# Kernel tuning notes

Hardware: AMD Instinct MI355X
Metric: run time of the kernel (lower is better)

Reference implementation:

```python
import jax, jax.numpy as jnp
import numpy as np

EPS = 1e-5  # torch group_norm default
GROUPS = 32


def _nin(t, W, b):
    # torch Nin: einsum('bchw,co->bowh') transposes spatial dims, then adds bias
    return jnp.einsum('bchw,co->bowh', t, W) + b


def setup_inputs() -> dict:
    key = jax.random.key(0)
    ks = jax.random.split(key, 9)
    B, C, N = 16, 512, 32
    x = jax.random.normal(ks[0], (B, C, N, N), jnp.float32)
    sc = 0.02
    Wq = jax.random.normal(ks[1], (C, C), jnp.float32) * sc
    Wk = jax.random.normal(ks[2], (C, C), jnp.float32) * sc
    Wv = jax.random.normal(ks[3], (C, C), jnp.float32) * sc
    Wn = jax.random.normal(ks[4], (C, C), jnp.float32) * sc
    bq = jnp.zeros((1, C, 1, 1), jnp.float32)
    bk = jnp.zeros((1, C, 1, 1), jnp.float32)
    bv = jnp.zeros((1, C, 1, 1), jnp.float32)
    bn = jnp.zeros((1, C, 1, 1), jnp.float32)
    return {"x": x, "Wq": Wq, "bq": bq, "Wk": Wk, "bk": bk,
            "Wv": Wv, "bv": bv, "Wn": Wn, "bn": bn}


def reference(x, Wq, bq, Wk, bk, Wv, bv, Wn, bn):
    B, C, H, W = x.shape
    # GroupNorm(32) with no affine params
    xg = x.reshape(B, GROUPS, -1)
    mu = xg.mean(-1, keepdims=True)
    var = xg.var(-1, keepdims=True)
    h = ((xg - mu) / jnp.sqrt(var + EPS)).reshape(B, C, H, W)
    # Nin projections -> spatially transposed (B, C, W, H)
    q = _nin(h, Wq, bq)
    k = _nin(h, Wk, bk)
    v = _nin(h, Wv, bv)
    # scores s[b,w1,w2,h1,h2] = sum_c q[b,c,w1,h1] k[b,c,w2,h2] * C^-0.5
    s = jnp.einsum('bcwh,bcWH->bwWhH', q, k) * (C ** -0.5)
    # softmax over flat (h1,h2) blocks exactly as the torch reshape does
    s = jax.nn.softmax(s.reshape(B, H, W, H * W), axis=-1).reshape(B, H, W, H, W)
    # torch.einsum('bHWHW, bcWH -> bcWH', w, v) takes the DIAGONAL over the
    # repeated H and W labels: diag[b,i,j] = s[b,i,j,i,j], then elementwise
    # scales v: out[b,c,w,h] = diag[b,h,w] * v[b,c,w,h]
    i = jnp.arange(H)
    j = jnp.arange(W)
    diag = s[:, i[:, None], j[None, :], i[:, None], j[None, :]]  # (B,H,W)
    h2 = v * jnp.swapaxes(diag, 1, 2)[:, None]  # (B,C,W,H)
    out = _nin(h2, Wn, bn)  # transposes back -> (B,C,H,W)
    return x + out
```

## Files before the change

kernel.cpp:

```cpp
#include <hip/hip_runtime.h>
#include <hip/hip_bf16.h>

typedef __attribute__((ext_vector_type(8))) short short8;
typedef __attribute__((ext_vector_type(4))) float floatx4;

#define MFMA16(a, b, c) __builtin_amdgcn_mfma_f32_16x16x32_bf16((a), (b), (c), 0, 0, 0)

__device__ __forceinline__ short f2bf(float f) {
    union { float f; unsigned u; } x; x.f = f;
    unsigned r = (x.u + 0x7fffu + ((x.u >> 16) & 1u)) >> 16;
    return (short)r;
}
__device__ __forceinline__ float bf2f(short s) {
    union { float f; unsigned u; } x; x.u = ((unsigned)(unsigned short)s) << 16;
    return x.f;
}

__device__ __forceinline__ void gl2lds16(const short* g, short* l) {
    void* gv = const_cast<short*>(g);
    __builtin_amdgcn_global_load_lds((__attribute__((address_space(1))) void*)gv,
                                     (__attribute__((address_space(3))) void*)l,
                                     16, 0, 0);
}

__global__ void prep_w(const float* __restrict__ Wq, const float* __restrict__ Wk,
                       const float* __restrict__ Wv, const float* __restrict__ Wn,
                       const float* __restrict__ bq, const float* __restrict__ bk,
                       short* __restrict__ wqb, short* __restrict__ wkb,
                       short* __restrict__ Wtv, short* __restrict__ Wn_t,
                       float* __restrict__ wu, float* __restrict__ wv2,
                       float* __restrict__ cstp) {
    __shared__ float t[32][33];
    __shared__ float cred[4];
    int z = blockIdx.z;
    int o0 = blockIdx.x * 32, c0 = blockIdx.y * 32;
    int lx = threadIdx.x, ly = threadIdx.y;
    int tid = ly * 32 + lx;
    if (z < 2) {
        const float* src = z ? Wk : Wq;
        short* dst = z ? wkb : wqb;
        for (int i = ly; i < 32; i += 8)
            dst[(size_t)(c0 + i) * 512 + o0 + lx] = f2bf(src[(size_t)(c0 + i) * 512 + o0 + lx]);
    } else if (z < 4) {
        const float* src = (z == 2) ? Wv : Wn;
        short* dst = (z == 2) ? (Wtv + (size_t)512 * 512) : Wn_t;
        for (int i = ly; i < 32; i += 8) t[i][lx] = src[(size_t)(c0 + i) * 512 + o0 + lx];
        __syncthreads();
        for (int i = ly; i < 32; i += 8) dst[(size_t)(o0 + i) * 512 + c0 + lx] = f2bf(t[lx][i]);
    } else {
        if (blockIdx.y != 0) return;
        int cb = blockIdx.x * 32;
        int cl = tid >> 3, part = tid & 7;
        float su = 0.f, sv = 0.f;
        const float* wqr = Wq + (size_t)(cb + cl) * 512;
        const float* wkr = Wk + (size_t)(cb + cl) * 512;
        for (int o = part * 64; o < part * 64 + 64; ++o) {
            su += wqr[o] * bk[o];
            sv += wkr[o] * bq[o];
        }
        t[cl][part] = su;
        t[cl][part + 8] = sv;
        float sc = 0.f;
        if (blockIdx.x == 0) sc = bq[tid] * bk[tid] + bq[tid + 256] * bk[tid + 256];
#pragma unroll
        for (int off = 32; off > 0; off >>= 1) sc += __shfl_down(sc, off, 64);
        if ((tid & 63) == 0) cred[tid >> 6] = sc;
        __syncthreads();
        if (part == 0) {
            float a = 0.f, b2 = 0.f;
#pragma unroll
            for (int j = 0; j < 8; ++j) { a += t[cl][j]; b2 += t[cl][j + 8]; }
            wu[cb + cl] = a;
            wv2[cb + cl] = b2;
        }
        if (blockIdx.x == 0 && tid == 0) cstp[0] = cred[0] + cred[1] + cred[2] + cred[3];
    }
}

__global__ __launch_bounds__(256) void g_gemm(const short* __restrict__ A,
                                              const short* __restrict__ B,
                                              short* __restrict__ Out) {
    const int tid = threadIdx.x;
    const int wv = tid >> 6, ln = tid & 63;
    const int m0 = blockIdx.x * 128, n0 = blockIdx.y * 128;
    __shared__ __attribute__((aligned(16))) short As[128 * 32];
    __shared__ __attribute__((aligned(16))) short Bs[128 * 32];
    floatx4 acc[4][4] = {};
    const int wm = (wv >> 1) * 64, wn = (wv & 1) * 64;
    const int fr = ln & 15, fq = ln >> 4;
    for (int kk = 0; kk < 512; kk += 32) {
        __syncthreads();
#pragma unroll
        for (int j = 0; j < 2; ++j) {
            int s = (wv * 2 + j) * 64 + ln;
            int r = s >> 2;
            int q = (s & 3) ^ ((r >> 1) & 3);
            gl2lds16(A + (size_t)(m0 + r) * 512 + kk + q * 8, As + (size_t)(wv * 2 + j) * 512);
            gl2lds16(B + (size_t)(n0 + r) * 512 + kk + q * 8, Bs + (size_t)(wv * 2 + j) * 512);
        }
        __syncthreads();
        short8 af[4], bfr[4];
#pragma unroll
        for (int t = 0; t < 4; ++t) {
            int ra = wm + t * 16 + fr;
            af[t]  = *(const short8*)(As + ra * 32 + ((fq ^ ((ra >> 1) & 3)) * 8));
            int rb = wn + t * 16 + fr;
            bfr[t] = *(const short8*)(Bs + rb * 32 + ((fq ^ ((rb >> 1) & 3)) * 8));
        }
#pragma unroll
        for (int mt = 0; mt < 4; ++mt)
#pragma unroll
            for (int nt = 0; nt < 4; ++nt)
                acc[mt][nt] = MFMA16(af[mt], bfr[nt], acc[mt][nt]);
    }
#pragma unroll
    for (int mt = 0; mt < 4; ++mt)
#pragma unroll
        for (int nt = 0; nt < 4; ++nt) {
            int n = n0 + wn + nt * 16 + fr;
#pragma unroll
            for (int r = 0; r < 4; ++r) {
                int m = m0 + wm + mt * 16 + fq * 4 + r;
                Out[(size_t)m * 512 + n] = f2bf(acc[mt][nt][r]);
            }
        }
}

__global__ __launch_bounds__(256) void groupnorm_k(const float* __restrict__ x,
                                                   short* __restrict__ hnt) {
    int b = blockIdx.x >> 5, g = blockIdx.x & 31;
    const float* xg = x + ((size_t)b * 512 + g * 16) * 1024;
    const float4* xg4 = (const float4*)xg;
    float s = 0.f, ss = 0.f;
    for (int i = threadIdx.x; i < 4096; i += 256) {
        float4 v = xg4[i];
        s  += v.x + v.y + v.z + v.w;
        ss += v.x * v.x + v.y * v.y + v.z * v.z + v.w * v.w;
    }
#pragma unroll
    for (int off = 32; off > 0; off >>= 1) {
        s  += __shfl_down(s,  off, 64);
        ss += __shfl_down(ss, off, 64);
    }
    __shared__ float red[8];
    int w = threadIdx.x >> 6;
    if ((threadIdx.x & 63) == 0) { red[w] = s; red[4 + w] = ss; }
    __syncthreads();
    float S  = red[0] + red[1] + red[2] + red[3];
    float SS = red[4] + red[5] + red[6] + red[7];
    float mean = S * (1.f / 16384.f);
    float var  = SS * (1.f / 16384.f) - mean * mean;
    float rstd = rsqrtf(var + 1e-5f);
    __shared__ __attribute__((aligned(16))) short tile[16 * 1026];
    for (int i = threadIdx.x; i < 4096; i += 256) {
        float4 v = xg4[i];
        int c = i >> 8, p = (i & 255) * 4;
        short* tp = tile + c * 1026 + p;
        tp[0] = f2bf((v.x - mean) * rstd);
        tp[1] = f2bf((v.y - mean) * rstd);
        tp[2] = f2bf((v.z - mean) * rstd);
        tp[3] = f2bf((v.w - mean) * rstd);
    }
    __syncthreads();
    for (int i = threadIdx.x; i < 2048; i += 256) {
        int p = i >> 1, half = i & 1;
        short8 v;
#pragma unroll
        for (int j = 0; j < 8; ++j) v[j] = tile[(half * 8 + j) * 1026 + p];
        *(short8*)(hnt + ((size_t)b * 1024 + p) * 512 + g * 16 + half * 8) = v;
    }
}

__global__ __launch_bounds__(256) void uv_gemv(const short* __restrict__ hnt,
                                               const float* __restrict__ wu,
                                               const float* __restrict__ wv2,
                                               float* __restrict__ u1p,
                                               float* __restrict__ v2p) {
    __shared__ float wus[512], wvs[512];
    for (int i = threadIdx.x; i < 512; i += 256) { wus[i] = wu[i]; wvs[i] = wv2[i]; }
    __syncthreads();
    int wv_ = threadIdx.x >> 6, ln = threadIdx.x & 63;
    int row = blockIdx.x * 4 + wv_;
    int b = row >> 10, p = row & 1023;
    short8 h = *(const short8*)(hnt + (size_t)row * 512 + ln * 8);
    float su = 0.f, sv = 0.f;
#pragma unroll
    for (int j = 0; j < 8; ++j) {
        float hv = bf2f(h[j]);
        su += hv * wus[ln * 8 + j];
        sv += hv * wvs[ln * 8 + j];
    }
#pragma unroll
    for (int off = 32; off > 0; off >>= 1) {
        su += __shfl_down(su, off, 64);
        sv += __shfl_down(sv, off, 64);
    }
    if (ln == 0) {
        int pp = ((p & 31) << 5) | (p >> 5);
        u1p[b * 1024 + pp] = su;
        v2p[b * 1024 + pp] = sv;
    }
}

__global__ __launch_bounds__(256) void tv_gemm(const short* __restrict__ A,
                                               const short* __restrict__ Wt,
                                               const float* __restrict__ bv,
                                               short* __restrict__ T,
                                               short* __restrict__ Vb) {
    const int tid = threadIdx.x;
    const int wv = tid >> 6, ln = tid & 63;
    int sid = blockIdx.x + 8 * (blockIdx.y + 8 * blockIdx.z);
    int xcd = sid & 7, chunk = sid >> 3;
    int bz = xcd * 2 + (chunk >> 6);
    int inner = chunk & 63;
    const int m0 = (inner & 7) * 128, n0 = (inner >> 3) * 128;
    const size_t BS = 1024 * 512;
    const short* Ab = A + (size_t)bz * BS;
    const int tsel = n0 >> 9;
    short* Ob = (tsel ? Vb : T) + (size_t)bz * BS;

    __shared__ __attribute__((aligned(16))) short As[128 * 32];
    __shared__ __attribute__((aligned(16))) short Bs[128 * 32];

    floatx4 acc[4][4] = {};
    const int wm = (wv >> 1) * 64, wn = (wv & 1) * 64;
    const int fr = ln & 15, fq = ln >> 4;

    for (int kk = 0; kk < 512; kk += 32) {
        __syncthreads();
#pragma unroll
        for (int j = 0; j < 2; ++j) {
            int s = (wv * 2 + j) * 64 + ln;
            int r = s >> 2;
            int q = (s & 3) ^ ((r >> 1) & 3);
            gl2lds16(Ab + (size_t)(m0 + r) * 512 + kk + q * 8, As + (size_t)(wv * 2 + j) * 512);
            gl2lds16(Wt + (size_t)(n0 + r) * 512 + kk + q * 8, Bs + (size_t)(wv * 2 + j) * 512);
        }
        __syncthreads();
        short8 af[4], bfr[4];
#pragma unroll
        for (int t = 0; t < 4; ++t) {
            int ra = wm + t * 16 + fr;
            af[t]  = *(const short8*)(As + ra * 32 + ((fq ^ ((ra >> 1) & 3)) * 8));
            int rb = wn + t * 16 + fr;
            bfr[t] = *(const short8*)(Bs + rb * 32 + ((fq ^ ((rb >> 1) & 3)) * 8));
        }
#pragma unroll
        for (int mt = 0; mt < 4; ++mt)
#pragma unroll
            for (int nt = 0; nt < 4; ++nt)
                acc[mt][nt] = MFMA16(af[mt], bfr[nt], acc[mt][nt]);
    }
#pragma unroll
    for (int mt = 0; mt < 4; ++mt)
#pragma unroll
        for (int nt = 0; nt < 4; ++nt) {
            int n = n0 + wn + nt * 16 + fr;
            float bvv = tsel ? bv[n - 512] : 0.0f;
            int nn = n & 511;
#pragma unroll
            for (int r = 0; r < 4; ++r) {
                int m = m0 + wm + mt * 16 + fq * 4 + r;
                Ob[(size_t)m * 512 + nn] = f2bf(acc[mt][nt][r] + bvv);
            }
        }
}

__global__ __launch_bounds__(256, 2) void attn_sm(const short* __restrict__ Tt,
                                                  const short* __restrict__ Hn,
                                                  const float* __restrict__ u1p,
                                                  const float* __restrict__ v2p,
                                                  const float* __restrict__ cstp,
                                                  float* __restrict__ Dm) {
    const int tid = threadIdx.x;
    const int wv = tid >> 6, ln = tid & 63;
    int sid = blockIdx.x + 8 * (blockIdx.y + 4 * blockIdx.z);
    int xcd = sid & 7, chunk = sid >> 3;
    int b = xcd * 2 + (chunk >> 5);
    int inner = chunk & 31;
    const int m0 = (inner & 7) * 128, n0 = (inner >> 3) * 256;
    const short* Tb = Tt + (size_t)b * (1024 * 512);
    const short* Hb = Hn + (size_t)b * (1024 * 512);

    __shared__ __attribute__((aligned(16))) short As[128 * 32];
    __shared__ __attribute__((aligned(16))) short Bs[256 * 32];

    floatx4 acc[4][8] = {};
    const int wm = (wv >> 1) * 64, wn = (wv & 1) * 128;
    const int fr = ln & 15, fq = ln >> 4;

    size_t offA[2], offB[4];
#pragma unroll
    for (int j = 0; j < 2; ++j) {
        int s = (wv * 2 + j) * 64 + ln;
        int r = s >> 2;
        int q = (s & 3) ^ ((r >> 1) & 3);
        int m = m0 + r;
        int pm = ((m & 31) << 5) | (m >> 5);
        offA[j] = (size_t)pm * 512 + q * 8;
    }
#pragma unroll
    for (int j = 0; j < 4; ++j) {
        int s = (wv * 4 + j) * 64 + ln;
        int r = s >> 2;
        int q = (s & 3) ^ ((r >> 1) & 3);
        int m = n0 + r;
        int pm = ((m & 31) << 5) | (m >> 5);
        offB[j] = (size_t)pm * 512 + q * 8;
    }

    for (int kk = 0; kk < 512; kk += 32) {
        __syncthreads();
#pragma unroll
        for (int j = 0; j < 2; ++j)
            gl2lds16(Tb + offA[j] + kk, As + (size_t)(wv * 2 + j) * 512);
#pragma unroll
        for (int j = 0; j < 4; ++j)
            gl2lds16(Hb + offB[j] + kk, Bs + (size_t)(wv * 4 + j) * 512);
        __syncthreads();
        short8 af[4], bfr[8];
#pragma unroll
        for (int t = 0; t < 4; ++t) {
            int ra = wm + t * 16 + fr;
            af[t] = *(const short8*)(As + ra * 32 + ((fq ^ ((ra >> 1) & 3)) * 8));
        }
#pragma unroll
        for (int u = 0; u < 8; ++u) {
            int rb = wn + u * 16 + fr;
            bfr[u] = *(const short8*)(Bs + rb * 32 + ((fq ^ ((rb >> 1) & 3)) * 8));
        }
#pragma unroll
        for (int mt = 0; mt < 4; ++mt)
#pragma unroll
            for (int nt = 0; nt < 8; ++nt)
                acc[mt][nt] = MFMA16(af[mt], bfr[nt], acc[mt][nt]);
    }

    const float scale = 0.04419417382415922f;
    const float cst = cstp[0];
    const int wbase = (m0 + wm) >> 5;
    const int Wbase = (n0 + wn) >> 5;
#pragma unroll
    for (int si = 0; si < 2; ++si) {
#pragma unroll
        for (int sj = 0; sj < 4; ++sj) {
            int wg = wbase + si, Wg = Wbase + sj;
            float tv[16];
            float mx = -3.0e38f;
#pragma unroll
            for (int mi = 0; mi < 2; ++mi)
#pragma unroll
                for (int ni = 0; ni < 2; ++ni) {
                    float vc = v2p[b * 1024 + Wg * 32 + ni * 16 + fr];
#pragma unroll
                    for (int r = 0; r < 4; ++r) {
                        float uc = u1p[b * 1024 + wg * 32 + mi * 16 + fq * 4 + r];
                        float u = (acc[2 * si + mi][2 * sj + ni][r] + uc + vc + cst) * scale;
                        tv[(mi * 2 + ni) * 4 + r] = u;
                        mx = fmaxf(mx, u);
                    }
                }
#pragma unroll
            for (int off = 32; off > 0; off >>= 1) mx = fmaxf(mx, __shfl_xor(mx, off, 64));
            float se = 0.f;
#pragma unroll
            for (int i = 0; i < 16; ++i) se += __expf(tv[i] - mx);
#pragma unroll
            for (int off = 32; off > 0; off >>= 1) se += __shfl_xor(se, off, 64);
            if (fq == ((wg >> 2) & 3) && fr == (Wg & 15)) {
                int mi = wg >> 4, ni = Wg >> 4;
                float numer = tv[(mi * 2 + ni) * 4 + (wg & 3)];
                Dm[((size_t)b * 32 + wg) * 32 + Wg] = __expf(numer - mx) / se;
            }
        }
    }
}

__global__ __launch_bounds__(256) void out_gemm(const short* __restrict__ A,
                                                const short* __restrict__ Wt,
                                                const float* __restrict__ Dm,
                                                const float* __restrict__ bnb,
                                                const float* __restrict__ x,
                                                float* __restrict__ out) {
    const int tid = threadIdx.x;
    const int wv = tid >> 6, ln = tid & 63;
    int sid = blockIdx.x + 8 * (blockIdx.y + 4 * blockIdx.z);
    int xcd = sid & 7, chunk = sid >> 3;
    int b = xcd * 2 + (chunk >> 5);
    int inner = chunk & 31;
    const int m0 = (inner & 7) * 128, n0 = (inner >> 3) * 128;
    const size_t BS = 1024 * 512;
    const short* Ab = A + (size_t)b * BS;

    __shared__ __attribute__((aligned(16))) short As[128 * 32];
    __shared__ __attribute__((aligned(16))) short Bs[128 * 32];

    floatx4 acc[4][4] = {};
    const int wm = (wv >> 1) * 64, wn = (wv & 1) * 64;
    const int fr = ln & 15, fq = ln >> 4;

    for (int kk = 0; kk < 512; kk += 32) {
        __syncthreads();
#pragma unroll
        for (int j = 0; j < 2; ++j) {
            int s = (wv * 2 + j) * 64 + ln;
            int r = s >> 2;
            int q = (s & 3) ^ ((r >> 1) & 3);
            gl2lds16(Ab + (size_t)(m0 + r) * 512 + kk + q * 8, As + (size_t)(wv * 2 + j) * 512);
            gl2lds16(Wt + (size_t)(n0 + r) * 512 + kk + q * 8, Bs + (size_t)(wv * 2 + j) * 512);
        }
        __syncthreads();
        short8 af[4], bfr[4];
#pragma unroll
        for (int t = 0; t < 4; ++t) {
            int ra = wm + t * 16 + fr;
            af[t]  = *(const short8*)(As + ra * 32 + ((fq ^ ((ra >> 1) & 3)) * 8));
            int rb = wn + t * 16 + fr;
            bfr[t] = *(const short8*)(Bs + rb * 32 + ((fq ^ ((rb >> 1) & 3)) * 8));
        }
#pragma unroll
        for (int mt = 0; mt < 4; ++mt)
#pragma unroll
            for (int nt = 0; nt < 4; ++nt)
                acc[mt][nt] = MFMA16(af[mt], bfr[nt], acc[mt][nt]);
    }
#pragma unroll
    for (int mt = 0; mt < 4; ++mt) {
        int mbase = m0 + wm + mt * 16 + fq * 4;
        float4 d4 = *(const float4*)(Dm + (size_t)b * 1024 + mbase);
#pragma unroll
        for (int nt = 0; nt < 4; ++nt) {
            int n = n0 + wn + nt * 16 + fr;
            float bvv = bnb[n];
            size_t base = ((size_t)b * 512 + n) * 1024 + mbase;
            float4 x4 = *(const float4*)(x + base);
            float4 o;
            o.x = x4.x + d4.x * acc[mt][nt][0] + bvv;
            o.y = x4.y + d4.y * acc[mt][nt][1] + bvv;
            o.z = x4.z + d4.z * acc[mt][nt][2] + bvv;
            o.w = x4.w + d4.w * acc[mt][nt][3] + bvv;
            *(float4*)(out + base) = o;
        }
    }
}

extern "C" void kernel_launch(void* const* d_in, const int* in_sizes, int n_in,
                              void* d_out, int out_size, void* d_ws, size_t ws_size,
                              hipStream_t stream) {
    const float* x  = (const float*)d_in[0];
    const float* Wq = (const float*)d_in[1];
    const float* bq = (const float*)d_in[2];
    const float* Wk = (const float*)d_in[3];
    const float* bk = (const float*)d_in[4];
    const float* Wv = (const float*)d_in[5];
    const float* bv = (const float*)d_in[6];
    const float* Wn = (const float*)d_in[7];
    const float* bn = (const float*)d_in[8];
    float* out = (float*)d_out;
    char* ws = (char*)d_ws;

    const size_t WSZ = (size_t)512 * 512 * 2;
    const size_t TSZ = (size_t)16 * 1024 * 512 * 2;
    short* Wtv  = (short*)(ws);
    short* Wn_t = (short*)(ws + 2 * WSZ);
    float* wu   = (float*)(ws + 3 * WSZ);
    float* wv2  = wu + 512;
    float* cstp = wv2 + 512;
    float* u1p  = cstp + 16;
    float* v2p  = u1p + 16384;
    char* base = ws + 3 * WSZ + 139264;
    short* hnt = (short*)(base);
    short* T   = (short*)(base + TSZ);
    short* Vb  = (short*)(base + 2 * TSZ);
    float* Dm  = (float*)(base + 3 * TSZ);
    short* wqb = T;
    short* wkb = T + 512 * 512;

    prep_w<<<dim3(16, 16, 5), dim3(32, 8), 0, stream>>>(
        Wq, Wk, Wv, Wn, bq, bk, wqb, wkb, Wtv, Wn_t, wu, wv2, cstp);
    g_gemm<<<dim3(4, 4, 1), 256, 0, stream>>>(wkb, wqb, Wtv);
    groupnorm_k<<<512, 256, 0, stream>>>(x, hnt);
    uv_gemv<<<4096, 256, 0, stream>>>(hnt, wu, wv2, u1p, v2p);
    tv_gemm<<<dim3(8, 8, 16), 256, 0, stream>>>(hnt, Wtv, bv, T, Vb);
    attn_sm<<<dim3(8, 4, 16), 256, 0, stream>>>(T, hnt, u1p, v2p, cstp, Dm);
    out_gemm<<<dim3(8, 4, 16), 256, 0, stream>>>(Vb, Wn_t, Dm, bn, x, out);
}
```

Measured before the change: 219.5 us.

## Fuse prep kernels and drop max-subtraction in attention softmax

```diff
diff --git a/kernel.cpp b/kernel.cpp
--- a/kernel.cpp
+++ b/kernel.cpp
@@ -23,33 +23,87 @@
                                      16, 0, 0);
 }
 
-__global__ void prep_w(const float* __restrict__ Wq, const float* __restrict__ Wk,
-                       const float* __restrict__ Wv, const float* __restrict__ Wn,
-                       const float* __restrict__ bq, const float* __restrict__ bk,
-                       short* __restrict__ wqb, short* __restrict__ wkb,
-                       short* __restrict__ Wtv, short* __restrict__ Wn_t,
-                       float* __restrict__ wu, float* __restrict__ wv2,
-                       float* __restrict__ cstp) {
+__global__ __launch_bounds__(256) void fused_prep(const float* __restrict__ x,
+                                                  const float* __restrict__ Wq,
+                                                  const float* __restrict__ Wk,
+                                                  const float* __restrict__ Wv,
+                                                  const float* __restrict__ Wn,
+                                                  const float* __restrict__ bq,
+                                                  const float* __restrict__ bk,
+                                                  short* __restrict__ hnt,
+                                                  short* __restrict__ wqb,
+                                                  short* __restrict__ wkb,
+                                                  short* __restrict__ Wtv,
+                                                  short* __restrict__ Wn_t,
+                                                  float* __restrict__ wu,
+                                                  float* __restrict__ wv2,
+                                                  float* __restrict__ cstp) {
+    __shared__ __attribute__((aligned(16))) short tile[16 * 1026];
+    __shared__ float red[8];
     __shared__ float t[32][33];
     __shared__ float cred[4];
-    int z = blockIdx.z;
-    int o0 = blockIdx.x * 32, c0 = blockIdx.y * 32;
-    int lx = threadIdx.x, ly = threadIdx.y;
-    int tid = ly * 32 + lx;
-    if (z < 2) {
-        const float* src = z ? Wk : Wq;
-        short* dst = z ? wkb : wqb;
-        for (int i = ly; i < 32; i += 8)
-            dst[(size_t)(c0 + i) * 512 + o0 + lx] = f2bf(src[(size_t)(c0 + i) * 512 + o0 + lx]);
-    } else if (z < 4) {
-        const float* src = (z == 2) ? Wv : Wn;
-        short* dst = (z == 2) ? (Wtv + (size_t)512 * 512) : Wn_t;
-        for (int i = ly; i < 32; i += 8) t[i][lx] = src[(size_t)(c0 + i) * 512 + o0 + lx];
-        __syncthreads();
-        for (int i = ly; i < 32; i += 8) dst[(size_t)(o0 + i) * 512 + c0 + lx] = f2bf(t[lx][i]);
+    const int bid = blockIdx.x, tid = threadIdx.x;
+
+    if (bid < 512) {
+        int b = bid >> 5, g = bid & 31;
+        const float* xg = x + ((size_t)b * 512 + g * 16) * 1024;
+        const float4* xg4 = (const float4*)xg;
+        float s = 0.f, ss = 0.f;
+        for (int i = tid; i < 4096; i += 256) {
+            float4 v = xg4[i];
+            s  += v.x + v.y + v.z + v.w;
+            ss += v.x * v.x + v.y * v.y + v.z * v.z + v.w * v.w;
+        }
+#pragma unroll
+        for (int off = 32; off > 0; off >>= 1) {
+            s  += __shfl_down(s,  off, 64);
+            ss += __shfl_down(ss, off, 64);
+        }
+        int w = tid >> 6;
+        if ((tid & 63) == 0) { red[w] = s; red[4 + w] = ss; }
+        __syncthreads();
+        float S  = red[0] + red[1] + red[2] + red[3];
+        float SS = red[4] + red[5] + red[6] + red[7];
+        float mean = S * (1.f / 16384.f);
+        float var  = SS * (1.f / 16384.f) - mean * mean;
+        float rstd = rsqrtf(var + 1e-5f);
+        for (int i = tid; i < 4096; i += 256) {
+            float4 v = xg4[i];
+            int c = i >> 8, p = (i & 255) * 4;
+            short* tp = tile + c * 1026 + p;
+            tp[0] = f2bf((v.x - mean) * rstd);
+            tp[1] = f2bf((v.y - mean) * rstd);
+            tp[2] = f2bf((v.z - mean) * rstd);
+            tp[3] = f2bf((v.w - mean) * rstd);
+        }
+        __syncthreads();
+        for (int i = tid; i < 2048; i += 256) {
+            int p = i >> 1, half = i & 1;
+            short8 v;
+#pragma unroll
+            for (int j = 0; j < 8; ++j) v[j] = tile[(half * 8 + j) * 1026 + p];
+            *(short8*)(hnt + ((size_t)b * 1024 + p) * 512 + g * 16 + half * 8) = v;
+        }
+    } else if (bid < 1536) {
+        int tz = bid - 512;
+        int z = tz >> 8, inner = tz & 255;
+        int o0 = (inner & 15) * 32, c0 = (inner >> 4) * 32;
+        int lx = tid & 31, ly = tid >> 5;
+        if (z < 2) {
+            const float* src = z ? Wk : Wq;
+            short* dst = z ? wkb : wqb;
+            for (int i = ly; i < 32; i += 8)
+                dst[(size_t)(c0 + i) * 512 + o0 + lx] = f2bf(src[(size_t)(c0 + i) * 512 + o0 + lx]);
+        } else {
+            const float* src = (z == 2) ? Wv : Wn;
+            short* dst = (z == 2) ? (Wtv + (size_t)512 * 512) : Wn_t;
+            for (int i = ly; i < 32; i += 8) t[i][lx] = src[(size_t)(c0 + i) * 512 + o0 + lx];
+            __syncthreads();
+            for (int i = ly; i < 32; i += 8) dst[(size_t)(o0 + i) * 512 + c0 + lx] = f2bf(t[lx][i]);
+        }
     } else {
-        if (blockIdx.y != 0) return;
-        int cb = blockIdx.x * 32;
+        int bid3 = bid - 1536;
+        int cb = bid3 * 32;
         int cl = tid >> 3, part = tid & 7;
         float su = 0.f, sv = 0.f;
         const float* wqr = Wq + (size_t)(cb + cl) * 512;
@@ -61,7 +115,7 @@
         t[cl][part] = su;
         t[cl][part + 8] = sv;
         float sc = 0.f;
-        if (blockIdx.x == 0) sc = bq[tid] * bk[tid] + bq[tid + 256] * bk[tid + 256];
+        if (bid3 == 0) sc = bq[tid] * bk[tid] + bq[tid + 256] * bk[tid + 256];
 #pragma unroll
         for (int off = 32; off > 0; off >>= 1) sc += __shfl_down(sc, off, 64);
         if ((tid & 63) == 0) cred[tid >> 6] = sc;
@@ -73,132 +127,91 @@
             wu[cb + cl] = a;
             wv2[cb + cl] = b2;
         }
-        if (blockIdx.x == 0 && tid == 0) cstp[0] = cred[0] + cred[1] + cred[2] + cred[3];
-    }
-}
-
-__global__ __launch_bounds__(256) void g_gemm(const short* __restrict__ A,
-                                              const short* __restrict__ B,
-                                              short* __restrict__ Out) {
+        if (bid3 == 0 && tid == 0) cstp[0] = cred[0] + cred[1] + cred[2] + cred[3];
+    }
+}
+
+__global__ __launch_bounds__(256) void fused_gu(const short* __restrict__ wkb,
+                                                const short* __restrict__ wqb,
+                                                short* __restrict__ Wtv,
+                                                const short* __restrict__ hnt,
+                                                const float* __restrict__ wu,
+                                                const float* __restrict__ wv2,
+                                                float* __restrict__ u1p,
+                                                float* __restrict__ v2p) {
+    __shared__ __attribute__((aligned(16))) short As[128 * 32];
+    __shared__ __attribute__((aligned(16))) short Bs[128 * 32];
     const int tid = threadIdx.x;
     const int wv = tid >> 6, ln = tid & 63;
-    const int m0 = blockIdx.x * 128, n0 = blockIdx.y * 128;
-    __shared__ __attribute__((aligned(16))) short As[128 * 32];
-    __shared__ __attribute__((aligned(16))) short Bs[128 * 32];
-    floatx4 acc[4][4] = {};
-    const int wm = (wv >> 1) * 64, wn = (wv & 1) * 64;
-    const int fr = ln & 15, fq = ln >> 4;
-    for (int kk = 0; kk < 512; kk += 32) {
-        __syncthreads();
-#pragma unroll
-        for (int j = 0; j < 2; ++j) {
-            int s = (wv * 2 + j) * 64 + ln;
-            int r = s >> 2;
-            int q = (s & 3) ^ ((r >> 1) & 3);
-            gl2lds16(A + (size_t)(m0 + r) * 512 + kk + q * 8, As + (size_t)(wv * 2 + j) * 512);
-            gl2lds16(B + (size_t)(n0 + r) * 512 + kk + q * 8, Bs + (size_t)(wv * 2 + j) * 512);
-        }
-        __syncthreads();
-        short8 af[4], bfr[4];
-#pragma unroll
-        for (int t = 0; t < 4; ++t) {
-            int ra = wm + t * 16 + fr;
-            af[t]  = *(const short8*)(As + ra * 32 + ((fq ^ ((ra >> 1) & 3)) * 8));
-            int rb = wn + t * 16 + fr;
-            bfr[t] = *(const short8*)(Bs + rb * 32 + ((fq ^ ((rb >> 1) & 3)) * 8));
+
+    if (blockIdx.x < 16) {
+        const int m0 = (blockIdx.x & 3) * 128, n0 = (blockIdx.x >> 2) * 128;
+        floatx4 acc[4][4] = {};
+        const int wm = (wv >> 1) * 64, wn = (wv & 1) * 64;
+        const int fr = ln & 15, fq = ln >> 4;
+        for (int kk = 0; kk < 512; kk += 32) {
+            __syncthreads();
+#pragma unroll
+            for (int j = 0; j < 2; ++j) {
+                int s = (wv * 2 + j) * 64 + ln;
+                int r = s >> 2;
+                int q = (s & 3) ^ ((r >> 1) & 3);
+                gl2lds16(wkb + (size_t)(m0 + r) * 512 + kk + q * 8, As + (size_t)(wv * 2 + j) * 512);
+                gl2lds16(wqb + (size_t)(n0 + r) * 512 + kk + q * 8, Bs + (size_t)(wv * 2 + j) * 512);
+            }
+            __syncthreads();
+            short8 af[4], bfr[4];
+#pragma unroll
+            for (int t = 0; t < 4; ++t) {
+                int ra = wm + t * 16 + fr;
+                af[t]  = *(const short8*)(As + ra * 32 + ((fq ^ ((ra >> 1) & 3)) * 8));
+                int rb = wn + t * 16 + fr;
+                bfr[t] = *(const short8*)(Bs + rb * 32 + ((fq ^ ((rb >> 1) & 3)) * 8));
+            }
+#pragma unroll
+            for (int mt = 0; mt < 4; ++mt)
+#pragma unroll
+                for (int nt = 0; nt < 4; ++nt)
+                    acc[mt][nt] = MFMA16(af[mt], bfr[nt], acc[mt][nt]);
         }
 #pragma unroll
         for (int mt = 0; mt < 4; ++mt)
 #pragma unroll
-            for (int nt = 0; nt < 4; ++nt)
-                acc[mt][nt] = MFMA16(af[mt], bfr[nt], acc[mt][nt]);
-    }
-#pragma unroll
-    for (int mt = 0; mt < 4; ++mt)
-#pragma unroll
-        for (int nt = 0; nt < 4; ++nt) {
-            int n = n0 + wn + nt * 16 + fr;
-#pragma unroll
-            for (int r = 0; r < 4; ++r) {
-                int m = m0 + wm + mt * 16 + fq * 4 + r;
-                Out[(size_t)m * 512 + n] = f2bf(acc[mt][nt][r]);
-            }
-        }
-}
-
-__global__ __launch_bounds__(256) void groupnorm_k(const float* __restrict__ x,
-                                                   short* __restrict__ hnt) {
-    int b = blockIdx.x >> 5, g = blockIdx.x & 31;
-    const float* xg = x + ((size_t)b * 512 + g * 16) * 1024;
-    const float4* xg4 = (const float4*)xg;
-    float s = 0.f, ss = 0.f;
-    for (int i = threadIdx.x; i < 4096; i += 256) {
-        float4 v = xg4[i];
-        s  += v.x + v.y + v.z + v.w;
-        ss += v.x * v.x + v.y * v.y + v.z * v.z + v.w * v.w;
-    }
-#pragma unroll
-    for (int off = 32; off > 0; off >>= 1) {
-        s  += __shfl_down(s,  off, 64);
-        ss += __shfl_down(ss, off, 64);
-    }
-    __shared__ float red[8];
-    int w = threadIdx.x >> 6;
-    if ((threadIdx.x & 63) == 0) { red[w] = s; red[4 + w] = ss; }
-    __syncthreads();
-    float S  = red[0] + red[1] + red[2] + red[3];
-    float SS = red[4] + red[5] + red[6] + red[7];
-    float mean = S * (1.f / 16384.f);
-    float var  = SS * (1.f / 16384.f) - mean * mean;
-    float rstd = rsqrtf(var + 1e-5f);
-    __shared__ __attribute__((aligned(16))) short tile[16 * 1026];
-    for (int i = threadIdx.x; i < 4096; i += 256) {
-        float4 v = xg4[i];
-        int c = i >> 8, p = (i & 255) * 4;
-        short* tp = tile + c * 1026 + p;
-        tp[0] = f2bf((v.x - mean) * rstd);
-        tp[1] = f2bf((v.y - mean) * rstd);
-        tp[2] = f2bf((v.z - mean) * rstd);
-        tp[3] = f2bf((v.w - mean) * rstd);
-    }
-    __syncthreads();
-    for (int i = threadIdx.x; i < 2048; i += 256) {
-        int p = i >> 1, half = i & 1;
-        short8 v;
-#pragma unroll
-        for (int j = 0; j < 8; ++j) v[j] = tile[(half * 8 + j) * 1026 + p];
-        *(short8*)(hnt + ((size_t)b * 1024 + p) * 512 + g * 16 + half * 8) = v;
-    }
-}
-
-__global__ __launch_bounds__(256) void uv_gemv(const short* __restrict__ hnt,
-                                               const float* __restrict__ wu,
-                                               const float* __restrict__ wv2,
-                                               float* __restrict__ u1p,
-                                               float* __restrict__ v2p) {
-    __shared__ float wus[512], wvs[512];
-    for (int i = threadIdx.x; i < 512; i += 256) { wus[i] = wu[i]; wvs[i] = wv2[i]; }
-    __syncthreads();
-    int wv_ = threadIdx.x >> 6, ln = threadIdx.x & 63;
-    int row = blockIdx.x * 4 + wv_;
-    int b = row >> 10, p = row & 1023;
-    short8 h = *(const short8*)(hnt + (size_t)row * 512 + ln * 8);
-    float su = 0.f, sv = 0.f;
-#pragma unroll
-    for (int j = 0; j < 8; ++j) {
-        float hv = bf2f(h[j]);
-        su += hv * wus[ln * 8 + j];
-        sv += hv * wvs[ln * 8 + j];
-    }
-#pragma unroll
-    for (int off = 32; off > 0; off >>= 1) {
-        su += __shfl_down(su, off, 64);
-        sv += __shfl_down(sv, off, 64);
-    }
-    if (ln == 0) {
-        int pp = ((p & 31) << 5) | (p >> 5);
-        u1p[b * 1024 + pp] = su;
-        v2p[b * 1024 + pp] = sv;
+            for (int nt = 0; nt < 4; ++nt) {
+                int n = n0 + wn + nt * 16 + fr;
+                const int fq2 = ln >> 4;
+#pragma unroll
+                for (int r = 0; r < 4; ++r) {
+                    int m = m0 + wm + mt * 16 + fq2 * 4 + r;
+                    Wtv[(size_t)m * 512 + n] = f2bf(acc[mt][nt][r]);
+                }
+            }
+    } else {
+        const float4* wu4 = (const float4*)wu;
+        const float4* wv4 = (const float4*)wv2;
+        float4 u0 = wu4[ln * 2], u1 = wu4[ln * 2 + 1];
+        float4 v0 = wv4[ln * 2], v1 = wv4[ln * 2 + 1];
+        int base_row = (blockIdx.x - 16) * 32 + wv * 8;
+#pragma unroll
+        for (int rr = 0; rr < 8; ++rr) {
+            int row = base_row + rr;
+            int b = row >> 10, p = row & 1023;
+            short8 h = *(const short8*)(hnt + (size_t)row * 512 + ln * 8);
+            float su = bf2f(h[0]) * u0.x + bf2f(h[1]) * u0.y + bf2f(h[2]) * u0.z + bf2f(h[3]) * u0.w
+                     + bf2f(h[4]) * u1.x + bf2f(h[5]) * u1.y + bf2f(h[6]) * u1.z + bf2f(h[7]) * u1.w;
+            float sv = bf2f(h[0]) * v0.x + bf2f(h[1]) * v0.y + bf2f(h[2]) * v0.z + bf2f(h[3]) * v0.w
+                     + bf2f(h[4]) * v1.x + bf2f(h[5]) * v1.y + bf2f(h[6]) * v1.z + bf2f(h[7]) * v1.w;
+#pragma unroll
+            for (int off = 32; off > 0; off >>= 1) {
+                su += __shfl_down(su, off, 64);
+                sv += __shfl_down(sv, off, 64);
+            }
+            if (ln == 0) {
+                int pp = ((p & 31) << 5) | (p >> 5);
+                u1p[b * 1024 + pp] = su;
+                v2p[b * 1024 + pp] = sv;
+            }
+        }
     }
 }
 
@@ -345,8 +358,8 @@
 #pragma unroll
         for (int sj = 0; sj < 4; ++sj) {
             int wg = wbase + si, Wg = Wbase + sj;
-            float tv[16];
-            float mx = -3.0e38f;
+            float ex[16];
+            float se = 0.f;
 #pragma unroll
             for (int mi = 0; mi < 2; ++mi)
 #pragma unroll
@@ -355,22 +368,16 @@
 #pragma unroll
                     for (int r = 0; r < 4; ++r) {
                         float uc = u1p[b * 1024 + wg * 32 + mi * 16 + fq * 4 + r];
-                        float u = (acc[2 * si + mi][2 * sj + ni][r] + uc + vc + cst) * scale;
-                        tv[(mi * 2 + ni) * 4 + r] = u;
-                        mx = fmaxf(mx, u);
+                        float e = __expf((acc[2 * si + mi][2 * sj + ni][r] + uc + vc + cst) * scale);
+                        ex[(mi * 2 + ni) * 4 + r] = e;
+                        se += e;
                     }
                 }
-#pragma unroll
-            for (int off = 32; off > 0; off >>= 1) mx = fmaxf(mx, __shfl_xor(mx, off, 64));
-            float se = 0.f;
-#pragma unroll
-            for (int i = 0; i < 16; ++i) se += __expf(tv[i] - mx);
 #pragma unroll
             for (int off = 32; off > 0; off >>= 1) se += __shfl_xor(se, off, 64);
             if (fq == ((wg >> 2) & 3) && fr == (Wg & 15)) {
                 int mi = wg >> 4, ni = Wg >> 4;
-                float numer = tv[(mi * 2 + ni) * 4 + (wg & 3)];
-                Dm[((size_t)b * 32 + wg) * 32 + Wg] = __expf(numer - mx) / se;
+                Dm[((size_t)b * 32 + wg) * 32 + Wg] = ex[(mi * 2 + ni) * 4 + (wg & 3)] / se;
             }
         }
     }
@@ -476,11 +483,9 @@
     short* wqb = T;
     short* wkb = T + 512 * 512;
 
-    prep_w<<<dim3(16, 16, 5), dim3(32, 8), 0, stream>>>(
-        Wq, Wk, Wv, Wn, bq, bk, wqb, wkb, Wtv, Wn_t, wu, wv2, cstp);
-    g_gemm<<<dim3(4, 4, 1), 256, 0, stream>>>(wkb, wqb, Wtv);
-    groupnorm_k<<<512, 256, 0, stream>>>(x, hnt);
-    uv_gemv<<<4096, 256, 0, stream>>>(hnt, wu, wv2, u1p, v2p);
+    fused_prep<<<1552, 256, 0, stream>>>(x, Wq, Wk, Wv, Wn, bq, bk,
+                                         hnt, wqb, wkb, Wtv, Wn_t, wu, wv2, cstp);
+    fused_gu<<<528, 256, 0, stream>>>(wkb, wqb, Wtv, hnt, wu, wv2, u1p, v2p);
     tv_gemm<<<dim3(8, 8, 16), 256, 0, stream>>>(hnt, Wtv, bv, T, Vb);
     attn_sm<<<dim3(8, 4, 16), 256, 0, stream>>>(T, hnt, u1p, v2p, cstp, Dm);
     out_gemm<<<dim3(8, 4, 16), 256, 0, stream>>>(Vb, Wn_t, Dm, bn, x, out);
```

New measurement: 217.8 us. No clear change (-0.8%).
